# Kernel optimization log

Hardware: AMD Instinct MI355X
Metric: run time of the kernel (lower is better)

## Reference

```python
import jax, jax.numpy as jnp
import numpy as np

EMBED_DIM = 1024
N_HEADS = 16
B, L = 2, 2048


def setup_inputs() -> dict:
    key = jax.random.key(0)
    ks = jax.random.split(key, 7)
    D = EMBED_DIM
    s = 1.0 / np.sqrt(D)
    return {
        "inputs": jax.random.normal(ks[0], (B, L, D), dtype=jnp.float32),
        "rotation_params": jax.random.normal(ks[1], (D, D), dtype=jnp.float32) * s,
        "entangle_params": jax.random.uniform(ks[2], (N_HEADS,), dtype=jnp.float32, minval=0.5, maxval=1.5),
        "Wq": jax.random.normal(ks[3], (D, D), dtype=jnp.float32) * s,
        "Wk": jax.random.normal(ks[4], (D, D), dtype=jnp.float32) * s,
        "Wv": jax.random.normal(ks[5], (D, D), dtype=jnp.float32) * s,
        "Wo": jax.random.normal(ks[6], (D, D), dtype=jnp.float32) * s,
    }


def reference(inputs, rotation_params, entangle_params, Wq, Wk, Wv, Wo):
    Bq, Lq, D = inputs.shape
    H = N_HEADS
    hd = D // H
    # Linear (no bias, torch convention x @ W.T) followed by rotation matmul
    Q = (inputs @ Wq.T) @ rotation_params
    K = (inputs @ Wk.T) @ rotation_params
    V = (inputs @ Wv.T) @ rotation_params
    # split heads: (B, H, L, hd)
    Q = Q.reshape(Bq, Lq, H, hd).transpose(0, 2, 1, 3)
    K = K.reshape(Bq, Lq, H, hd).transpose(0, 2, 1, 3)
    V = V.reshape(Bq, Lq, H, hd).transpose(0, 2, 1, 3)
    scale = entangle_params.reshape(1, H, 1, 1) / jnp.sqrt(jnp.asarray(hd, dtype=inputs.dtype))
    scores = jnp.einsum("bhqd,bhkd->bhqk", Q, K) * scale
    attn = jax.nn.softmax(scores, axis=-1)  # dropout inert (eval / p=0)
    out = jnp.einsum("bhqk,bhkd->bhqd", attn, V)
    out = out.transpose(0, 2, 1, 3).reshape(Bq, Lq, D)
    return out @ Wo.T
```

## Files before the change

kernel.cpp:

```cpp
#include <hip/hip_runtime.h>
#include <cstdint>
#include <cstddef>

typedef __attribute__((ext_vector_type(8))) short  bf16x8;
typedef __attribute__((ext_vector_type(8))) _Float16 f16x8;
typedef __attribute__((ext_vector_type(4))) _Float16 f16x4;
typedef __attribute__((ext_vector_type(4))) float  f32x4;
typedef __attribute__((ext_vector_type(4))) unsigned short u16x4;
typedef __attribute__((ext_vector_type(2))) unsigned int u32x2;

#define LOG2E 1.44269504088896340736f
#define PBIAS 6.0f

__device__ __forceinline__ unsigned short f2bf(float f) {
  unsigned int u = __builtin_bit_cast(unsigned int, f);
  u += 0x7fffu + ((u >> 16) & 1u);
  return (unsigned short)(u >> 16);
}
__device__ __forceinline__ float bf2f(unsigned short s) {
  unsigned int u = ((unsigned int)s) << 16;
  return __builtin_bit_cast(float, u);
}

__device__ __forceinline__ float fast_exp2(float x) {
  return __builtin_amdgcn_exp2f(x);
}

__device__ __forceinline__ void gll16(const void* g, void* l) {
  __builtin_amdgcn_global_load_lds(
      (const __attribute__((address_space(1))) unsigned int*)g,
      (__attribute__((address_space(3))) unsigned int*)l, 16, 0, 0);
}

__global__ __launch_bounds__(256) void prep(
    const float* __restrict__ x,  unsigned short* __restrict__ xb,
    const float* __restrict__ Wo, unsigned short* __restrict__ Wob,
    const float* __restrict__ R,  const float* __restrict__ Wq,
    const float* __restrict__ Wk, const float* __restrict__ Wv,
    unsigned short* __restrict__ RT,  unsigned short* __restrict__ WqT,
    unsigned short* __restrict__ WkT, unsigned short* __restrict__ WvT) {
  int bid = blockIdx.x;
  __shared__ unsigned short s[64][68];
  if (bid < 5120) {
    const float* src = bid < 4096 ? x : Wo;
    unsigned short* dst = bid < 4096 ? xb : Wob;
    int i = (bid < 4096 ? bid : bid - 4096) * 256 + threadIdx.x;
    float4 v = ((const float4*)src)[i];
    u16x4 o;
    o[0] = f2bf(v.x); o[1] = f2bf(v.y); o[2] = f2bf(v.z); o[3] = f2bf(v.w);
    ((u16x4*)dst)[i] = o;
    return;
  }
  int t = bid - 5120;
  int z = t >> 8, tile = t & 255;
  const float* in = z == 0 ? R : (z == 1 ? Wq : (z == 2 ? Wk : Wv));
  unsigned short* out = z == 0 ? RT : (z == 1 ? WqT : (z == 2 ? WkT : WvT));
  int r0 = (tile >> 4) * 64, c0 = (tile & 15) * 64;
  int tt = threadIdx.x;
  int tr = tt >> 4, tc4 = (tt & 15) * 4;
  for (int i = 0; i < 4; ++i) {
    int r = tr + i * 16;
    float4 v = *(const float4*)(in + (size_t)(r0 + r) * 1024 + c0 + tc4);
    s[r][tc4 + 0] = f2bf(v.x); s[r][tc4 + 1] = f2bf(v.y);
    s[r][tc4 + 2] = f2bf(v.z); s[r][tc4 + 3] = f2bf(v.w);
  }
  __syncthreads();
  for (int i = 0; i < 4; ++i) {
    int oc = tr + i * 16;
    u16x4 o;
    o[0] = s[tc4 + 0][oc]; o[1] = s[tc4 + 1][oc];
    o[2] = s[tc4 + 2][oc]; o[3] = s[tc4 + 3][oc];
    *(u16x4*)(out + (size_t)(c0 + oc) * 1024 + r0 + tc4) = o;
  }
}

__global__ void tr_v(const unsigned short* __restrict__ in, unsigned short* __restrict__ out) {
  __shared__ unsigned short s[64][68];
  int t = threadIdx.x;
  int r0 = blockIdx.y * 64, c0 = blockIdx.x * 64;
  int tr = t >> 4, tc4 = (t & 15) * 4;
  for (int i = 0; i < 4; ++i) {
    int r = tr + i * 16;
    u16x4 v = *(const u16x4*)(in + (size_t)(r0 + r) * 1024 + c0 + tc4);
    s[r][tc4 + 0] = v[0]; s[r][tc4 + 1] = v[1]; s[r][tc4 + 2] = v[2]; s[r][tc4 + 3] = v[3];
  }
  __syncthreads();
  for (int i = 0; i < 4; ++i) {
    int oc = tr + i * 16;
    u16x4 o;
#pragma unroll
    for (int j = 0; j < 4; ++j) {
      _Float16 h = (_Float16)bf2f(s[tc4 + j][oc]);
      o[j] = __builtin_bit_cast(unsigned short, h);
    }
    int col = r0 + tc4;
    int c32 = col & 31;
    int pos = (col & ~31) + ((c32 >> 2) & 3) * 8 + (c32 >> 4) * 4;
    *(u16x4*)(out + (size_t)(c0 + oc) * 4096 + pos) = o;
  }
}

template <bool BF16OUT>
__global__ __launch_bounds__(256) void gemm_nt(
    const unsigned short* __restrict__ A,
    const unsigned short* __restrict__ B0, const unsigned short* __restrict__ B1,
    const unsigned short* __restrict__ B2,
    void* __restrict__ C0, void* __restrict__ C1, void* __restrict__ C2,
    int M, int N, int K) {
  const unsigned short* B = blockIdx.z == 0 ? B0 : (blockIdx.z == 1 ? B1 : B2);
  void* Cv = blockIdx.z == 0 ? C0 : (blockIdx.z == 1 ? C1 : C2);

  __shared__ unsigned short As[2][128 * 64];
  __shared__ unsigned short Bs[2][128 * 64];

  int tid = threadIdx.x, w = tid >> 6, lane = tid & 63;
  int lo = lane & 15, quad = lane >> 4;
  int m0 = blockIdx.y * 128, n0 = blockIdx.x * 128;
  int wm = (w >> 1) * 64, wn = (w & 1) * 64;

  f32x4 z4 = {0.f, 0.f, 0.f, 0.f};
  f32x4 acc[4][4];
  for (int mi = 0; mi < 4; ++mi)
    for (int ni = 0; ni < 4; ++ni) acc[mi][ni] = z4;

  int rloc = lane >> 3;
  int srcChunk = (lane & 7) ^ (rloc & 7);
  int cbase = w * 4;
  const unsigned short* Ag = A + (size_t)(m0 + cbase * 8 + rloc) * K + srcChunk * 8;
  const unsigned short* Bg = B + (size_t)(n0 + cbase * 8 + rloc) * K + srcChunk * 8;
  int ldsOfs = cbase * 512 + lane * 8;
  int cx0 = (quad ^ (lane & 7)) * 8;
  int cx1 = ((quad + 4) ^ (lane & 7)) * 8;

#pragma unroll
  for (int j = 0; j < 4; ++j) {
    gll16(Ag + (size_t)j * 8 * K, As[0] + ldsOfs + j * 512);
    gll16(Bg + (size_t)j * 8 * K, Bs[0] + ldsOfs + j * 512);
  }

  int nk = K >> 6;
  for (int kt = 0; kt < nk; ++kt) {
    int buf = kt & 1;
    __syncthreads();
    if (kt + 1 < nk) {
      int k0 = (kt + 1) << 6;
#pragma unroll
      for (int j = 0; j < 4; ++j) {
        gll16(Ag + (size_t)j * 8 * K + k0, As[buf ^ 1] + ldsOfs + j * 512);
        gll16(Bg + (size_t)j * 8 * K + k0, Bs[buf ^ 1] + ldsOfs + j * 512);
      }
    }
    const unsigned short* Ab = As[buf];
    const unsigned short* Bb = Bs[buf];
#pragma unroll
    for (int ks = 0; ks < 2; ++ks) {
      int cx = ks ? cx1 : cx0;
      bf16x8 af[4], bfr[4];
#pragma unroll
      for (int mi = 0; mi < 4; ++mi)
        af[mi] = *(const bf16x8*)(Ab + (wm + mi * 16 + lo) * 64 + cx);
#pragma unroll
      for (int ni = 0; ni < 4; ++ni)
        bfr[ni] = *(const bf16x8*)(Bb + (wn + ni * 16 + lo) * 64 + cx);
#pragma unroll
      for (int mi = 0; mi < 4; ++mi)
#pragma unroll
        for (int ni = 0; ni < 4; ++ni)
          acc[mi][ni] = __builtin_amdgcn_mfma_f32_16x16x32_bf16(af[mi], bfr[ni], acc[mi][ni], 0, 0, 0);
    }
  }

#pragma unroll
  for (int mi = 0; mi < 4; ++mi)
#pragma unroll
    for (int ni = 0; ni < 4; ++ni)
      for (int i = 0; i < 4; ++i) {
        int r = m0 + wm + mi * 16 + quad * 4 + i;
        int c = n0 + wn + ni * 16 + lo;
        if (BF16OUT)
          ((unsigned short*)Cv)[(size_t)r * N + c] = f2bf(acc[mi][ni][i]);
        else
          ((float*)Cv)[(size_t)r * N + c] = acc[mi][ni][i];
      }
}

__global__ __launch_bounds__(512, 4) void flash_attn(
    const unsigned short* __restrict__ Q, const unsigned short* __restrict__ Kg_,
    const unsigned short* __restrict__ Vt, const float* __restrict__ ent,
    unsigned short* __restrict__ O) {
  int tid = threadIdx.x, w = tid >> 6, lane = tid & 63;
  int lo = lane & 15, quad = lane >> 4;
  int half = w >> 2, wl = w & 3;

  int bid = blockIdx.x;
  int g = (bid & 7) + 8 * (bid >> 7);
  int qt = (bid >> 3) & 15;
  int b = g >> 4, h = g & 15;
  int q0 = qt * 128;
  float scale = ent[h] * (0.125f * LOG2E);

  __shared__ unsigned short lds[32768];

  bf16x8 aq[2][2];
#pragma unroll
  for (int f = 0; f < 2; ++f)
#pragma unroll
    for (int ks = 0; ks < 2; ++ks) {
      uint4 v = *(const uint4*)(Q + (size_t)(b * 2048 + q0 + wl * 32 + f * 16 + lo) * 1024 +
                                h * 64 + ks * 32 + quad * 8);
      unsigned int* pv = (unsigned int*)&v;
      uint4 o; unsigned int* po = (unsigned int*)&o;
#pragma unroll
      for (int j = 0; j < 4; ++j) {
        float f0 = bf2f((unsigned short)(pv[j] & 0xffffu)) * scale;
        float f1 = bf2f((unsigned short)(pv[j] >> 16)) * scale;
        po[j] = (unsigned int)f2bf(f0) | ((unsigned int)f2bf(f1) << 16);
      }
      aq[f][ks] = *(bf16x8*)&o;
    }

  f32x4 binit = {-PBIAS, -PBIAS, -PBIAS, -PBIAS};
  f32x4 z4 = {0.f, 0.f, 0.f, 0.f};
  f32x4 acco[4][2];
#pragma unroll
  for (int di = 0; di < 4; ++di) {
    acco[di][0] = z4; acco[di][1] = z4;
  }
  float lsum0 = 0.f, lsum1 = 0.f;

  int rloc = lane >> 3;
  int srcChunk = (lane & 7) ^ (rloc & 7);
  int cb = wl * 2;
  const unsigned short* Kp = Kg_ + (size_t)(b * 2048 + half * 1024) * 1024 + h * 64;
  const unsigned short* Vp = Vt + (size_t)(h * 64) * 4096 + (size_t)(b * 2048 + half * 1024);
  int cx0 = (quad ^ (lane & 7)) * 8;
  int cx1 = ((quad + 4) ^ (lane & 7)) * 8;

  unsigned short* Kh = lds + half * 2 * 4096;
  unsigned short* Vh = lds + 16384 + half * 2 * 4096;

#pragma unroll
  for (int j = 0; j < 2; ++j) {
    int c = cb + j;
    int r = c * 8 + rloc;
    gll16(Kp + (size_t)r * 1024 + srcChunk * 8, Kh + c * 512 + lane * 8);
    gll16(Vp + (size_t)r * 4096 + srcChunk * 8, Vh + c * 512 + lane * 8);
  }

  for (int it = 0; it < 16; ++it) {
    int buf = it & 1;
    __syncthreads();
    if (it + 1 < 16) {
      int kvn = (it + 1) * 64;
#pragma unroll
      for (int j = 0; j < 2; ++j) {
        int c = cb + j;
        int r = c * 8 + rloc;
        gll16(Kp + (size_t)(kvn + r) * 1024 + srcChunk * 8, Kh + (buf ^ 1) * 4096 + c * 512 + lane * 8);
        gll16(Vp + (size_t)r * 4096 + kvn + srcChunk * 8, Vh + (buf ^ 1) * 4096 + c * 512 + lane * 8);
      }
    }
    const unsigned short* Kb_ = Kh + buf * 4096;
    const unsigned short* Vb_ = Vh + buf * 4096;

    f32x4 accs[4][2];
    __builtin_amdgcn_s_setprio(1);
#pragma unroll
    for (int kt = 0; kt < 4; ++kt) {
      bf16x8 kf0 = *(const bf16x8*)(Kb_ + (kt * 16 + lo) * 64 + cx0);
      bf16x8 kf1 = *(const bf16x8*)(Kb_ + (kt * 16 + lo) * 64 + cx1);
#pragma unroll
      for (int f = 0; f < 2; ++f) {
        f32x4 a = __builtin_amdgcn_mfma_f32_16x16x32_bf16(kf0, aq[f][0], binit, 0, 0, 0);
        accs[kt][f] = __builtin_amdgcn_mfma_f32_16x16x32_bf16(kf1, aq[f][1], a, 0, 0, 0);
      }
    }
    __builtin_amdgcn_s_setprio(0);

    f16x4 ap[4][2];
#pragma unroll
    for (int kt = 0; kt < 4; ++kt) {
#pragma unroll
      for (int f = 0; f < 2; ++f) {
        float p0 = fast_exp2(accs[kt][f][0]);
        float p1 = fast_exp2(accs[kt][f][1]);
        float p2 = fast_exp2(accs[kt][f][2]);
        float p3 = fast_exp2(accs[kt][f][3]);
        if (f == 0) lsum0 += (p0 + p1) + (p2 + p3);
        else        lsum1 += (p0 + p1) + (p2 + p3);
        u32x2 uu;
        uu[0] = __builtin_bit_cast(unsigned int, __builtin_amdgcn_cvt_pkrtz(p0, p1));
        uu[1] = __builtin_bit_cast(unsigned int, __builtin_amdgcn_cvt_pkrtz(p2, p3));
        ap[kt][f] = __builtin_bit_cast(f16x4, uu);
      }
    }

    __builtin_amdgcn_s_setprio(1);
#pragma unroll
    for (int t2 = 0; t2 < 2; ++t2) {
      f16x8 a80 = __builtin_shufflevector(ap[2 * t2][0], ap[2 * t2 + 1][0], 0, 1, 2, 3, 4, 5, 6, 7);
      f16x8 a81 = __builtin_shufflevector(ap[2 * t2][1], ap[2 * t2 + 1][1], 0, 1, 2, 3, 4, 5, 6, 7);
#pragma unroll
      for (int di = 0; di < 4; ++di) {
        f16x8 bv8 = *(const f16x8*)(Vb_ + (di * 16 + lo) * 64 +
                                    (((t2 * 4 + quad) ^ (lo & 7)) << 3));
        acco[di][0] = __builtin_amdgcn_mfma_f32_16x16x32_f16(a80, bv8, acco[di][0], 0, 0, 0);
        acco[di][1] = __builtin_amdgcn_mfma_f32_16x16x32_f16(a81, bv8, acco[di][1], 0, 0, 0);
      }
    }
    __builtin_amdgcn_s_setprio(0);
  }

  __syncthreads();
  float* cm = (float*)lds;
  float* base = cm + wl * 2304;
  if (half == 1) {
#pragma unroll
    for (int di = 0; di < 4; ++di)
#pragma unroll
      for (int f = 0; f < 2; ++f)
#pragma unroll
        for (int i = 0; i < 4; ++i)
          base[(di * 8 + f * 4 + i) * 64 + lane] = acco[di][f][i];
    base[32 * 64 + lane] = lsum0;
    base[33 * 64 + lane] = lsum1;
  }
  __syncthreads();
  if (half == 1) return;

#pragma unroll
  for (int di = 0; di < 4; ++di)
#pragma unroll
    for (int f = 0; f < 2; ++f)
#pragma unroll
      for (int i = 0; i < 4; ++i)
        acco[di][f][i] += base[(di * 8 + f * 4 + i) * 64 + lane];
  lsum0 += base[32 * 64 + lane];
  lsum1 += base[33 * 64 + lane];

#pragma unroll
  for (int f = 0; f < 2; ++f) {
    float v = f == 0 ? lsum0 : lsum1;
    v += __shfl_xor(v, 16);
    v += __shfl_xor(v, 32);
    float inv = 1.0f / v;

#pragma unroll
    for (int i = 0; i < 4; ++i) {
      float invq = __shfl(inv, quad * 4 + i);
#pragma unroll
      for (int di = 0; di < 4; ++di) {
        size_t ofs = (size_t)(b * 2048 + q0 + wl * 32 + f * 16 + quad * 4 + i) * 1024 +
                     h * 64 + di * 16 + lo;
        O[ofs] = f2bf(acco[di][f][i] * invq);
      }
    }
  }
}

extern "C" void kernel_launch(void* const* d_in, const int* in_sizes, int n_in,
                              void* d_out, int out_size, void* d_ws, size_t ws_size,
                              hipStream_t stream) {
  const float* x   = (const float*)d_in[0];
  const float* R   = (const float*)d_in[1];
  const float* ent = (const float*)d_in[2];
  const float* Wq  = (const float*)d_in[3];
  const float* Wk  = (const float*)d_in[4];
  const float* Wv  = (const float*)d_in[5];
  const float* Wo  = (const float*)d_in[6];
  float* out = (float*)d_out;

  const size_t MLD = (size_t)4096 * 1024;
  const size_t DD  = (size_t)1024 * 1024;
  if (ws_size < (MLD * 6 + DD * 8) * 2) return;

  unsigned short* ws  = (unsigned short*)d_ws;
  unsigned short* xb  = ws;
  unsigned short* RT  = xb + MLD;
  unsigned short* WqT = RT + DD;
  unsigned short* WkT = WqT + DD;
  unsigned short* WvT = WkT + DD;
  unsigned short* Wob = WvT + DD;
  unsigned short* AqT = Wob + DD;
  unsigned short* AkT = AqT + DD;
  unsigned short* AvT = AkT + DD;
  unsigned short* Qb  = AvT + DD;
  unsigned short* Kb  = Qb + MLD;
  unsigned short* Vb  = Kb + MLD;
  unsigned short* Vtf = Vb + MLD;
  unsigned short* aO  = Vtf + MLD;

  prep<<<dim3(6144), dim3(256), 0, stream>>>(
      x, xb, Wo, Wob, R, Wq, Wk, Wv, RT, WqT, WkT, WvT);

  gemm_nt<true><<<dim3(8, 8, 3), dim3(256), 0, stream>>>(
      RT, WqT, WkT, WvT, (void*)AqT, (void*)AkT, (void*)AvT, 1024, 1024, 1024);
  gemm_nt<true><<<dim3(8, 32, 3), dim3(256), 0, stream>>>(
      xb, AqT, AkT, AvT, (void*)Qb, (void*)Kb, (void*)Vb, 4096, 1024, 1024);
  tr_v<<<dim3(16, 64), dim3(256), 0, stream>>>(Vb, Vtf);
  flash_attn<<<dim3(512), dim3(512), 0, stream>>>(Qb, Kb, Vtf, ent, aO);
  gemm_nt<false><<<dim3(8, 32, 1), dim3(256), 0, stream>>>(
      aO, Wob, Wob, Wob, (void*)out, (void*)out, (void*)out, 4096, 1024, 1024);
}
```

Measured before the change: 205.9 us.

## Fuse Q/K/V projection GEMMs into one kernel sharing the A tile

Adds a gemm_qkv kernel in which each block loads one 128x64 tile of x and multiplies it against the three projection weight tiles, so three accumulator sets are computed from one A load instead of three separate z-slices. This removes two thirds of the A-side global and LDS traffic for the QKV projection. In exchange the block count drops from 768 to 256 and register and LDS use per block rise sharply (48 accumulator tiles, 128KB of LDS), so occupancy falls. The output GEMM also swaps its grid mapping so blockIdx.x walks M, which changes block scheduling order for cache locality.

Result: no change. 206.8 us (+0.4%).

```diff
diff --git a/kernel.cpp b/kernel.cpp
--- a/kernel.cpp
+++ b/kernel.cpp
@@ -100,7 +100,7 @@
   }
 }
 
-template <bool BF16OUT>
+template <bool BF16OUT, bool SWAP>
 __global__ __launch_bounds__(256) void gemm_nt(
     const unsigned short* __restrict__ A,
     const unsigned short* __restrict__ B0, const unsigned short* __restrict__ B1,
@@ -115,7 +115,8 @@
 
   int tid = threadIdx.x, w = tid >> 6, lane = tid & 63;
   int lo = lane & 15, quad = lane >> 4;
-  int m0 = blockIdx.y * 128, n0 = blockIdx.x * 128;
+  int m0 = (SWAP ? blockIdx.x : blockIdx.y) * 128;
+  int n0 = (SWAP ? blockIdx.y : blockIdx.x) * 128;
   int wm = (w >> 1) * 64, wn = (w & 1) * 64;
 
   f32x4 z4 = {0.f, 0.f, 0.f, 0.f};
@@ -182,6 +183,105 @@
         else
           ((float*)Cv)[(size_t)r * N + c] = acc[mi][ni][i];
       }
+}
+
+__global__ __launch_bounds__(256, 1) void gemm_qkv(
+    const unsigned short* __restrict__ A,
+    const unsigned short* __restrict__ B0, const unsigned short* __restrict__ B1,
+    const unsigned short* __restrict__ B2,
+    unsigned short* __restrict__ C0, unsigned short* __restrict__ C1,
+    unsigned short* __restrict__ C2,
+    int M, int N, int K) {
+  __shared__ unsigned short As[2][128 * 64];
+  __shared__ unsigned short Bs[2][3][128 * 64];
+
+  int tid = threadIdx.x, w = tid >> 6, lane = tid & 63;
+  int lo = lane & 15, quad = lane >> 4;
+  int m0 = blockIdx.x * 128, n0 = blockIdx.y * 128;
+  int wm = (w >> 1) * 64, wn = (w & 1) * 64;
+
+  f32x4 z4 = {0.f, 0.f, 0.f, 0.f};
+  f32x4 acc[3][4][4];
+#pragma unroll
+  for (int z = 0; z < 3; ++z)
+#pragma unroll
+    for (int mi = 0; mi < 4; ++mi)
+#pragma unroll
+      for (int ni = 0; ni < 4; ++ni) acc[z][mi][ni] = z4;
+
+  int rloc = lane >> 3;
+  int srcChunk = (lane & 7) ^ (rloc & 7);
+  int cbase = w * 4;
+  const unsigned short* Ag = A + (size_t)(m0 + cbase * 8 + rloc) * K + srcChunk * 8;
+  size_t bofs = (size_t)(n0 + cbase * 8 + rloc) * K + srcChunk * 8;
+  const unsigned short* Bg0 = B0 + bofs;
+  const unsigned short* Bg1 = B1 + bofs;
+  const unsigned short* Bg2 = B2 + bofs;
+  int ldsOfs = cbase * 512 + lane * 8;
+  int cx0 = (quad ^ (lane & 7)) * 8;
+  int cx1 = ((quad + 4) ^ (lane & 7)) * 8;
+
+#pragma unroll
+  for (int j = 0; j < 4; ++j) {
+    gll16(Ag  + (size_t)j * 8 * K, As[0]    + ldsOfs + j * 512);
+    gll16(Bg0 + (size_t)j * 8 * K, Bs[0][0] + ldsOfs + j * 512);
+    gll16(Bg1 + (size_t)j * 8 * K, Bs[0][1] + ldsOfs + j * 512);
+    gll16(Bg2 + (size_t)j * 8 * K, Bs[0][2] + ldsOfs + j * 512);
+  }
+
+  int nk = K >> 6;
+  for (int kt = 0; kt < nk; ++kt) {
+    int buf = kt & 1;
+    __syncthreads();
+    if (kt + 1 < nk) {
+      int k0 = (kt + 1) << 6;
+#pragma unroll
+      for (int j = 0; j < 4; ++j) {
+        gll16(Ag  + (size_t)j * 8 * K + k0, As[buf ^ 1]    + ldsOfs + j * 512);
+        gll16(Bg0 + (size_t)j * 8 * K + k0, Bs[buf ^ 1][0] + ldsOfs + j * 512);
+        gll16(Bg1 + (size_t)j * 8 * K + k0, Bs[buf ^ 1][1] + ldsOfs + j * 512);
+        gll16(Bg2 + (size_t)j * 8 * K + k0, Bs[buf ^ 1][2] + ldsOfs + j * 512);
+      }
+    }
+    const unsigned short* Ab = As[buf];
+#pragma unroll
+    for (int ks = 0; ks < 2; ++ks) {
+      int cx = ks ? cx1 : cx0;
+      bf16x8 af[4];
+#pragma unroll
+      for (int mi = 0; mi < 4; ++mi)
+        af[mi] = *(const bf16x8*)(Ab + (wm + mi * 16 + lo) * 64 + cx);
+#pragma unroll
+      for (int z = 0; z < 3; ++z) {
+        const unsigned short* Bb = Bs[buf][z];
+        bf16x8 bfr[4];
+#pragma unroll
+        for (int ni = 0; ni < 4; ++ni)
+          bfr[ni] = *(const bf16x8*)(Bb + (wn + ni * 16 + lo) * 64 + cx);
+#pragma unroll
+        for (int mi = 0; mi < 4; ++mi)
+#pragma unroll
+          for (int ni = 0; ni < 4; ++ni)
+            acc[z][mi][ni] = __builtin_amdgcn_mfma_f32_16x16x32_bf16(af[mi], bfr[ni], acc[z][mi][ni], 0, 0, 0);
+      }
+    }
+  }
+
+  unsigned short* Cz0 = C0; unsigned short* Cz1 = C1; unsigned short* Cz2 = C2;
+#pragma unroll
+  for (int z = 0; z < 3; ++z) {
+    unsigned short* Cv = z == 0 ? Cz0 : (z == 1 ? Cz1 : Cz2);
+#pragma unroll
+    for (int mi = 0; mi < 4; ++mi)
+#pragma unroll
+      for (int ni = 0; ni < 4; ++ni)
+#pragma unroll
+        for (int i = 0; i < 4; ++i) {
+          int r = m0 + wm + mi * 16 + quad * 4 + i;
+          int c = n0 + wn + ni * 16 + lo;
+          Cv[(size_t)r * N + c] = f2bf(acc[z][mi][ni][i]);
+        }
+  }
 }
 
 __global__ __launch_bounds__(512, 4) void flash_attn(
@@ -393,12 +493,12 @@
   prep<<<dim3(6144), dim3(256), 0, stream>>>(
       x, xb, Wo, Wob, R, Wq, Wk, Wv, RT, WqT, WkT, WvT);
 
-  gemm_nt<true><<<dim3(8, 8, 3), dim3(256), 0, stream>>>(
+  gemm_nt<true, false><<<dim3(8, 8, 3), dim3(256), 0, stream>>>(
       RT, WqT, WkT, WvT, (void*)AqT, (void*)AkT, (void*)AvT, 1024, 1024, 1024);
-  gemm_nt<true><<<dim3(8, 32, 3), dim3(256), 0, stream>>>(
-      xb, AqT, AkT, AvT, (void*)Qb, (void*)Kb, (void*)Vb, 4096, 1024, 1024);
+  gemm_qkv<<<dim3(32, 8), dim3(256), 0, stream>>>(
+      xb, AqT, AkT, AvT, Qb, Kb, Vb, 4096, 1024, 1024);
   tr_v<<<dim3(16, 64), dim3(256), 0, stream>>>(Vb, Vtf);
   flash_attn<<<dim3(512), dim3(512), 0, stream>>>(Qb, Kb, Vtf, ent, aO);
-  gemm_nt<false><<<dim3(8, 32, 1), dim3(256), 0, stream>>>(
+  gemm_nt<false, true><<<dim3(32, 8, 1), dim3(256), 0, stream>>>(
       aO, Wob, Wob, Wob, (void*)out, (void*)out, (void*)out, 4096, 1024, 1024);
 }
```
